# Optimization experiments

Hardware: AMD Instinct MI355X
Metric: run time of the kernel (lower is better)

## Reference

```python
import jax, jax.numpy as jnp
import numpy as np

N_NODES = 4096
JACOBI_ITERS = 10
EPS = 1e-5


def sym_laplacian_dense(edge_index, n):
    # L = I - D^{-1/2} A D^{-1/2}, duplicates in edge_index accumulate (as scipy COO does)
    row, col = edge_index[0], edge_index[1]
    A = jnp.zeros((n, n), jnp.float32).at[row, col].add(1.0)
    deg = A.sum(axis=1)
    dinv = jnp.where(deg > 0, 1.0 / jnp.sqrt(jnp.where(deg > 0, deg, 1.0)), 0.0)
    return jnp.eye(n, dtype=jnp.float32) - dinv[:, None] * A * dinv[None, :]


def jacobi_eig(a, iterations):
    # Faithful Jacobi: `iterations` Givens rotations, each zeroing the max |off-diag| entry.
    n = a.shape[0]
    upper = jnp.triu(jnp.ones((n, n), bool), k=1)

    def body(_, carry):
        a, p = carry
        idx = jnp.argmax(jnp.where(upper, jnp.abs(a), 0.0))
        k, l = idx // n, idx % n
        akl = a[k, l]
        aDiff = a[l, l] - a[k, k]
        akl_safe = jnp.where(akl == 0.0, 1.0, akl)
        aDiff_safe = jnp.where(aDiff == 0.0, 1.0, aDiff)
        phi = aDiff / (2.0 * akl_safe)
        t2 = 1.0 / (jnp.abs(phi) + jnp.sqrt(phi * phi + 1.0))
        t2 = jnp.where(phi < 0.0, -t2, t2)
        t1 = akl / aDiff_safe
        t = jnp.where(jnp.abs(akl) < jnp.abs(aDiff) * 1e-36, t1, t2)
        c = 1.0 / jnp.sqrt(t * t + 1.0)
        s = t * c
        # a <- G^T a G  (equivalent to the triangular in-place updates for symmetric a)
        ck, cl = a[:, k], a[:, l]
        a = a.at[:, k].set(c * ck - s * cl).at[:, l].set(s * ck + c * cl)
        rk, rl = a[k, :], a[l, :]
        a = a.at[k, :].set(c * rk - s * rl).at[l, :].set(s * rk + c * rl)
        a = a.at[k, l].set(0.0).at[l, k].set(0.0)
        pk, pl = p[:, k], p[:, l]
        p = p.at[:, k].set(c * pk - s * pl).at[:, l].set(s * pk + c * pl)
        return a, p

    a, p = jax.lax.fori_loop(0, iterations, body, (a, jnp.eye(n, dtype=a.dtype)))
    return jnp.diagonal(a), p


def setup_inputs() -> dict:
    key = jax.random.key(0)
    ks = jax.random.split(key, 8)
    n, cin, cout, r, e = N_NODES, 64, 64, 4, 100000
    x = jax.random.normal(ks[0], (n, cin), jnp.float32)
    src = jax.random.randint(ks[1], (e,), 0, n)
    dst = jax.random.randint(ks[2], (e,), 0, n)
    # symmetric graph (undirected), as the Jacobi solver assumes a symmetric Laplacian
    edge_index = jnp.stack([jnp.concatenate([src, dst]), jnp.concatenate([dst, src])]).astype(jnp.int64)
    stdv = 1.0 / np.sqrt(cin)
    real_weight = jax.random.uniform(ks[3], (cout, cin, r, 1), jnp.float32, -stdv, stdv)
    imag_weight = jax.random.uniform(ks[4], (cout, cin, r, 1), jnp.float32, -stdv, stdv)
    h = jax.random.uniform(ks[5], (cout, cin), jnp.float32, -stdv, stdv)
    c = jax.random.uniform(ks[6], (cout, cin, 1), jnp.float32, -stdv, stdv)
    bias = jnp.zeros((cout,), jnp.float32)
    return {"x": x, "edge_index": edge_index, "real_weight": real_weight,
            "imag_weight": imag_weight, "h": h, "c": c, "bias": bias}


def reference(x, edge_index, real_weight, imag_weight, h, c, bias):
    n = x.shape[0]
    r = real_weight.shape[2]
    L = sym_laplacian_dense(edge_index, n)
    w, U = jacobi_eig(L, JACOBI_ITERS)          # w: (N,), U: (N, N)
    aux = U.T @ x                                # (N, in)
    hw = h[:, :, None] * w[None, None, :]        # (out, in, N)
    a2 = jnp.where(hw > EPS,
                   2.0 * jnp.arctan(1.0 / jnp.where(hw > EPS, hw, 1.0)),
                   2.0)
    # theta[o,i,j,n] = a2[o,i,n] * (j+1)  -> (out, in, r, N)
    theta = a2[:, :, None, :] * jnp.arange(1, r + 1, dtype=x.dtype)[None, None, :, None]
    g = real_weight * jnp.cos(theta) - imag_weight * jnp.sin(theta)
    g = g.sum(axis=2) + c                        # (out, in, N)
    out = jnp.einsum('oin,ni->on', g, aux)       # Pmul + sum over in-channels
    output = U @ out.T + bias                    # (N, out); note: original's clamp(min=0) is a no-op
    return output
```

## Files before the change

### kernel.cpp

```cpp
#include <hip/hip_runtime.h>
#include <hip/hip_bf16.h>

#pragma clang fp contract(off)

#define N 4096
#define CIN 64
#define COUT 64
#define ITERS 10
#define MAXS 32
#define CANDMAX 384

typedef unsigned long long u64;

__device__ __forceinline__ u64 packkey(float v, unsigned j) {
    return ((u64)__float_as_uint(v) << 32) | (u64)(~j);
}
__device__ __forceinline__ u64 gkey(unsigned vb, unsigned row, unsigned col) {
    unsigned flat = (row << 12) | col;
    return ((u64)vb << 24) | (u64)((~flat) & 0xFFFFFFu);
}

__global__ void init_prep_k(int* __restrict__ deg, int* __restrict__ fill,
                            const float* __restrict__ hh, const float* __restrict__ cw,
                            const float* __restrict__ rw, const float* __restrict__ iw,
                            float2* __restrict__ hcT, float4* __restrict__ rwT,
                            float4* __restrict__ iwT) {
    int b = blockIdx.x;
    if (b < 16) {
        int i = b * 256 + threadIdx.x;
        deg[i] = 0; fill[i] = 0;
    } else {
        int idx = (b - 16) * 256 + threadIdx.x;
        int i = idx >> 6, o = idx & 63;
        int src = o * 64 + i;
        hcT[idx] = make_float2(hh[src], cw[src]);
        rwT[idx] = make_float4(rw[src * 4 + 0], rw[src * 4 + 1], rw[src * 4 + 2], rw[src * 4 + 3]);
        iwT[idx] = make_float4(iw[src * 4 + 0], iw[src * 4 + 1], iw[src * 4 + 2], iw[src * 4 + 3]);
    }
}

__global__ void edges1_k(const int* __restrict__ ei, int* __restrict__ deg, int E) {
    int e = blockIdx.x * 256 + threadIdx.x;
    if (e < E) atomicAdd(&deg[ei[e]], 1);
}

__global__ void __launch_bounds__(1024) scan_k(const int* __restrict__ deg,
                                               int* __restrict__ rowptr,
                                               float* __restrict__ dinv) {
    __shared__ int ps[1024];
    int t = threadIdx.x, b = t * 4;
    int d0 = deg[b], d1 = deg[b + 1], d2 = deg[b + 2], d3 = deg[b + 3];
    int local = d0 + d1 + d2 + d3;
    ps[t] = local;
    __syncthreads();
    for (int off = 1; off < 1024; off <<= 1) {
        int v = (t >= off) ? ps[t - off] : 0;
        __syncthreads();
        ps[t] += v;
        __syncthreads();
    }
    int excl = ps[t] - local;
    rowptr[b] = excl; rowptr[b + 1] = excl + d0;
    rowptr[b + 2] = excl + d0 + d1; rowptr[b + 3] = excl + d0 + d1 + d2;
    if (t == 1023) rowptr[4096] = ps[1023];
    dinv[b]     = d0 > 0 ? 1.0f / sqrtf((float)d0) : 0.0f;
    dinv[b + 1] = d1 > 0 ? 1.0f / sqrtf((float)d1) : 0.0f;
    dinv[b + 2] = d2 > 0 ? 1.0f / sqrtf((float)d2) : 0.0f;
    dinv[b + 3] = d3 > 0 ? 1.0f / sqrtf((float)d3) : 0.0f;
}

__global__ void edges2_k(const int* __restrict__ ei, const int* __restrict__ rowptr,
                         int* __restrict__ fill, int* __restrict__ colidx, int E) {
    int e = blockIdx.x * 256 + threadIdx.x;
    if (e < E) {
        int r = ei[e], c = ei[E + e];
        int pos = rowptr[r] + atomicAdd(&fill[r], 1);
        colidx[pos] = c;
    }
}

__global__ void __launch_bounds__(64) rowmax0_k(
        const int* __restrict__ rowptr, const int* __restrict__ colidx,
        const float* __restrict__ dinv, const float* __restrict__ x,
        float* __restrict__ y, float* __restrict__ diag, u64* __restrict__ top24T) {
    const int i = blockIdx.x, t = threadIdx.x;
    __shared__ float row[N];
    __shared__ u64 cand[CANDMAX];
    __shared__ int scnt;
    int rs = rowptr[i], re = rowptr[i + 1];
    if (t == 0) { scnt = 0; row[i] = 0.0f; }
    __syncthreads();
    for (int e = rs + t; e < re; e += 64) { int c2 = colidx[e]; if (c2 >= i) row[c2] = 0.0f; }
    __syncthreads();
    for (int e = rs + t; e < re; e += 64) { int c2 = colidx[e]; if (c2 >= i) atomicAdd(&row[c2], 1.0f); }
    __syncthreads();
    float di = dinv[i];
    for (int e = rs + t; e < re; e += 64) {
        int c2 = colidx[e];
        if (c2 > i) {
            float v = -((di * row[c2]) * dinv[c2]);
            int idx = atomicAdd(&scnt, 1);
            if (idx < CANDMAX) cand[idx] = packkey(fabsf(v), (unsigned)c2);
        }
    }
    __syncthreads();
    int L = scnt < CANDMAX ? scnt : CANDMAX;
    for (int r = 0; r < 24; ++r) {
        u64 best = 0ull;
        for (int idx = t; idx < L; idx += 64) { u64 cc = cand[idx]; if (cc > best) best = cc; }
        for (int off = 32; off; off >>= 1) { u64 o = __shfl_xor(best, off, 64); if (o > best) best = o; }
        if (t == 0) top24T[(size_t)r * N + i] = best;
        for (int idx = t; idx < L; idx += 64) { if (cand[idx] == best) cand[idx] = 0ull; }
        __syncthreads();
    }
    if (t == 0) diag[i] = 1.0f - ((di * row[i]) * di);
    y[i * CIN + t] = x[i * CIN + t];
}

__global__ void __launch_bounds__(1024) jacobi_k(
        const int* __restrict__ rowptr, const int* __restrict__ colidx,
        const float* __restrict__ dinv,
        float* __restrict__ diag, const u64* __restrict__ top24T, float* __restrict__ y,
        float* __restrict__ rowS, float* __restrict__ colS,
        int* __restrict__ dslotG, int* __restrict__ slistG, int* __restrict__ nslotsG,
        int* __restrict__ rotk, int* __restrict__ rotl,
        float* __restrict__ rotc, float* __restrict__ rotsv) {
    __shared__ __align__(16) float cntK[N], cntL[N];
    __shared__ __align__(16) float rowKst[N], rowLst[N];
    __shared__ __align__(16) float dinvL[N];
    __shared__ u64 rmaxL[N];
    __shared__ float rvalL[N];
    __shared__ float diagL[N];
    __shared__ short dslotL[N];
    __shared__ u64 rmaxSlot[MAXS];
    __shared__ u64 w16[16], w16b[16];
    __shared__ float ovRowK[MAXS], ovRowL[MAXS], ovColK[MAXS], ovColL[MAXS];
    __shared__ int slistL[MAXS];
    __shared__ unsigned short sdirty[64];
    __shared__ int S_snd;
    const int t = threadIdx.x;

    u64 mb0 = 0ull;
    for (int i = t; i < N; i += 1024) {
        u64 kk = top24T[i];
        rmaxL[i] = kk;
        rvalL[i] = -__uint_as_float((unsigned)(kk >> 32));
        diagL[i] = diag[i];
        dinvL[i] = dinv[i];
        dslotL[i] = -1;
        unsigned col = (~(unsigned)kk) & 4095u;
        u64 gk = gkey((unsigned)(kk >> 32), (unsigned)i, col);
        if (gk > mb0) mb0 = gk;
    }
    for (int off = 32; off; off >>= 1) { u64 o = __shfl_down(mb0, off, 64); if (o > mb0) mb0 = o; }
    if ((t & 63) == 0) w16[t >> 6] = mb0;
    __syncthreads();
    u64 pivot = w16[0];
    for (int w = 1; w < 16; ++w) if (w16[w] > pivot) pivot = w16[w];
    int nsCur = 0;

    for (int it = 0; it < ITERS; ++it) {
        unsigned flat = (~(unsigned)pivot) & 0xFFFFFFu;
        const int k = (int)(flat >> 12), l = (int)(flat & 4095u);
        const float akl = rvalL[k];
        const float akk = diagL[k], all_ = diagL[l];
        float aDiff = all_ - akk;
        float akl_safe = (akl == 0.0f) ? 1.0f : akl;
        float aDiff_safe = (aDiff == 0.0f) ? 1.0f : aDiff;
        float phi = aDiff / (2.0f * akl_safe);
        float t2 = 1.0f / (fabsf(phi) + sqrtf(phi * phi + 1.0f));
        t2 = (phi < 0.0f) ? -t2 : t2;
        float t1 = akl / aDiff_safe;
        float tt = (fabsf(akl) < fabsf(aDiff) * 1e-36f) ? t1 : t2;
        const float c = 1.0f / sqrtf(tt * tt + 1.0f);
        const float s = tt * c;
        float a1kk = c * akk - s * akl;
        float a1kl = s * akk + c * akl;
        float a1lk = c * akl - s * all_;
        float a1ll = s * akl + c * all_;
        const float a2kk = c * a1kk - s * a1lk;
        const float a2ll = s * a1kl + c * a1ll;
        int ok = dslotL[k], ol = dslotL[l];
        const int nold = nsCur;
        const bool freshK = (ok < 0), freshL = (ol < 0);
        int sk2 = ok, sl3 = ol;
        { int ns = nsCur; if (freshK) sk2 = ns++; if (freshL) sl3 = ns++; nsCur = ns; }
        const int slotk = sk2, slotl = sl3;
        const float dk = dinvL[k], dl = dinvL[l];
        if (freshK) for (int j = t; j < N; j += 1024) cntK[j] = 0.0f;
        if (freshL) for (int j = t; j < N; j += 1024) cntL[j] = 0.0f;
        __syncthreads();
        if (t == 0) {
            rotk[it] = k; rotl[it] = l; rotc[it] = c; rotsv[it] = s;
            diagL[k] = a2kk; diagL[l] = a2ll;
            if (freshK) { slistL[slotk] = k; dslotL[k] = (short)slotk; }
            if (freshL) { slistL[slotl] = l; dslotL[l] = (short)slotl; }
            S_snd = 0;
        }
        if (t < CIN) {
            float yk = y[k * CIN + t], yl = y[l * CIN + t];
            y[k * CIN + t] = c * yk - s * yl;
            y[l * CIN + t] = s * yk + c * yl;
        }
        if (t >= 64 && t < 64 + nold) {
            int sl2 = t - 64;
            if (freshK) { ovRowK[sl2] = colS[(size_t)sl2 * N + k]; ovColK[sl2] = rowS[(size_t)sl2 * N + k]; }
            if (freshL) { ovRowL[sl2] = colS[(size_t)sl2 * N + l]; ovColL[sl2] = rowS[(size_t)sl2 * N + l]; }
        }
        if (freshK) for (int e = rowptr[k] + t; e < rowptr[k + 1]; e += 1024) atomicAdd(&cntK[colidx[e]], 1.0f);
        if (freshL) for (int e = rowptr[l] + t; e < rowptr[l + 1]; e += 1024) atomicAdd(&cntL[colidx[e]], 1.0f);
        __syncthreads();
        u64 bk = packkey(0.0f, 4095u), bl = packkey(0.0f, 4095u);
        {
            const int j0 = t * 4;
            float4 dj4 = *reinterpret_cast<const float4*>(dinvL + j0);
            float4 bK4, bL4, cK4, cL4;
            if (freshK) {
                float4 cnt = *reinterpret_cast<const float4*>(cntK + j0);
#pragma unroll
                for (int m = 0; m < 4; ++m) {
                    float cn = (&cnt.x)[m], dj = (&dj4.x)[m];
                    (&bK4.x)[m] = -((dk * cn) * dj);
                    (&cK4.x)[m] = -((dj * cn) * dk);
                }
            } else {
                bK4 = *reinterpret_cast<const float4*>(rowS + (size_t)ok * N + j0);
                cK4 = *reinterpret_cast<const float4*>(colS + (size_t)ok * N + j0);
            }
            if (freshL) {
                float4 cnt = *reinterpret_cast<const float4*>(cntL + j0);
#pragma unroll
                for (int m = 0; m < 4; ++m) {
                    float cn = (&cnt.x)[m], dj = (&dj4.x)[m];
                    (&bL4.x)[m] = -((dl * cn) * dj);
                    (&cL4.x)[m] = -((dj * cn) * dl);
                }
            } else {
                bL4 = *reinterpret_cast<const float4*>(rowS + (size_t)ol * N + j0);
                cL4 = *reinterpret_cast<const float4*>(colS + (size_t)ol * N + j0);
            }
            float4 nrK4, nrL4, ncK4, ncL4;
#pragma unroll
            for (int m = 0; m < 4; ++m) {
                int j = j0 + m;
                float bK = (&bK4.x)[m], bL = (&bL4.x)[m];
                float cK = (&cK4.x)[m], cL = (&cL4.x)[m];
                float nrk, nrl, nck, ncl;
                if (j == k)      { nrk = a2kk; nrl = 0.0f; nck = a2kk; ncl = 0.0f; }
                else if (j == l) { nrk = 0.0f; nrl = a2ll; nck = 0.0f; ncl = a2ll; }
                else {
                    int sl2 = dslotL[j];
                    if (sl2 >= 0 && sl2 < nold) {
                        if (freshK) { bK = ovRowK[sl2]; cK = ovColK[sl2]; }
                        if (freshL) { bL = ovRowL[sl2]; cL = ovColL[sl2]; }
                    }
                    nrk = c * bK - s * bL; nrl = s * bK + c * bL;
                    nck = c * cK - s * cL; ncl = s * cK + c * cL;
                }
                (&nrK4.x)[m] = nrk; (&nrL4.x)[m] = nrl;
                (&ncK4.x)[m] = nck; (&ncL4.x)[m] = ncl;
                if (j > k) { u64 kk = packkey(fabsf(nrk), (unsigned)j); if (kk > bk) bk = kk; }
                if (j > l) { u64 kk = packkey(fabsf(nrl), (unsigned)j); if (kk > bl) bl = kk; }
            }
            *reinterpret_cast<float4*>(rowS + (size_t)slotk * N + j0) = nrK4;
            *reinterpret_cast<float4*>(rowS + (size_t)slotl * N + j0) = nrL4;
            *reinterpret_cast<float4*>(colS + (size_t)slotk * N + j0) = ncK4;
            *reinterpret_cast<float4*>(colS + (size_t)slotl * N + j0) = ncL4;
            *reinterpret_cast<float4*>(rowKst + j0) = nrK4;
            *reinterpret_cast<float4*>(rowLst + j0) = nrL4;
            *reinterpret_cast<float4*>(cntK + j0) = ncK4;
            *reinterpret_cast<float4*>(cntL + j0) = ncL4;
        }
        for (int off = 32; off; off >>= 1) {
            u64 o = __shfl_down(bk, off, 64); if (o > bk) bk = o;
            u64 o2 = __shfl_down(bl, off, 64); if (o2 > bl) bl = o2;
        }
        if ((t & 63) == 0) { w16[t >> 6] = bk; w16b[t >> 6] = bl; }
        __syncthreads();
        if (t == 0) {
            u64 b1 = w16[0], b2 = w16b[0];
            for (int w = 1; w < 16; ++w) { if (w16[w] > b1) b1 = w16[w]; if (w16b[w] > b2) b2 = w16b[w]; }
            unsigned j1 = (~(unsigned)b1) & 4095u, j2 = (~(unsigned)b2) & 4095u;
            rvalL[k] = rowKst[j1];
            rvalL[l] = rowLst[j2];
            rmaxSlot[slotk] = gkey((unsigned)(b1 >> 32), (unsigned)k, j1);
            rmaxSlot[slotl] = gkey((unsigned)(b2 >> 32), (unsigned)l, j2);
        }
        if (t >= 64 && t < 64 + nold) {
            int sl2 = t - 64;
            int js = slistL[sl2];
            if (js != k && js != l) {
                float vkj = rowKst[js];
                float vlj = rowLst[js];
                float vjk = cntK[js];
                float vjl = cntL[js];
                colS[(size_t)sl2 * N + k] = vkj;
                colS[(size_t)sl2 * N + l] = vlj;
                rowS[(size_t)sl2 * N + k] = vjk;
                rowS[(size_t)sl2 * N + l] = vjl;
                u64 cached = rmaxSlot[sl2];
                unsigned cj = ((~(unsigned)cached) & 0xFFFFFFu) & 4095u;
                bool kc = (k > js), lc = (l > js);
                u64 ck2 = kc ? gkey(__float_as_uint(fabsf(vjk)), (unsigned)js, (unsigned)k) : 0ull;
                u64 cl2 = lc ? gkey(__float_as_uint(fabsf(vjl)), (unsigned)js, (unsigned)l) : 0ull;
                bool stale = false; u64 base = cached; bool useOld = true;
                if (kc && cj == (unsigned)k)      { if (ck2 < cached) stale = true; else { base = 0ull; useOld = false; } }
                else if (lc && cj == (unsigned)l) { if (cl2 < cached) stale = true; else { base = 0ull; useOld = false; } }
                if (!stale) {
                    if (kc || lc) {
                        u64 mm = base; float mv = useOld ? rvalL[js] : 0.0f;
                        if (ck2 > mm) { mm = ck2; mv = vjk; }
                        if (cl2 > mm) { mm = cl2; mv = vjl; }
                        rmaxSlot[sl2] = mm; rvalL[js] = mv;
                    }
                } else { int d2 = atomicAdd(&S_snd, 1); sdirty[d2] = (unsigned short)sl2; }
            }
        }
        u64 myBest = 0ull;
#pragma unroll
        for (int m = 0; m < 4; ++m) {
            int j = t + 1024 * m;
            if (dslotL[j] >= 0) continue;
            float nck = cntK[j], ncl = cntL[j];
            u64 cached = rmaxL[j];
            unsigned cj = (~(unsigned)cached) & 4095u;
            bool kc = (k > j), lc = (l > j);
            u64 ck2 = kc ? packkey(fabsf(nck), (unsigned)k) : 0ull;
            u64 cl2 = lc ? packkey(fabsf(ncl), (unsigned)l) : 0ull;
            bool stale = false; u64 base = cached; bool useOld = true;
            if (kc && cj == (unsigned)k)      { if (ck2 < cached) stale = true; else { base = 0ull; useOld = false; } }
            else if (lc && cj == (unsigned)l) { if (cl2 < cached) stale = true; else { base = 0ull; useOld = false; } }
            if (!stale) {
                if (kc || lc) {
                    u64 mm = base; float mv = useOld ? rvalL[j] : 0.0f;
                    if (ck2 > mm) { mm = ck2; mv = nck; }
                    if (cl2 > mm) { mm = cl2; mv = ncl; }
                    rmaxL[j] = mm; rvalL[j] = mv;
                }
            } else {
                u64 bKey = 0ull; float bVal = 0.0f;
                for (int cc = 0; cc < 24; ++cc) {
                    u64 cand = top24T[(size_t)cc * N + j];
                    unsigned col = (~(unsigned)cand) & 4095u;
                    if (dslotL[col] < 0) {
                        bKey = cand;
                        bVal = -__uint_as_float((unsigned)(cand >> 32));
                        break;
                    }
                }
                for (int sl = 0; sl < nsCur; ++sl) {
                    if (sl == slotk || sl == slotl) continue;
                    int js = slistL[sl];
                    if (js > j) {
                        float v = colS[(size_t)sl * N + j];
                        u64 kk2 = packkey(fabsf(v), (unsigned)js);
                        if (kk2 > bKey) { bKey = kk2; bVal = v; }
                    }
                }
                if (kc && ck2 > bKey) { bKey = ck2; bVal = nck; }
                if (lc && cl2 > bKey) { bKey = cl2; bVal = ncl; }
                rmaxL[j] = bKey; rvalL[j] = bVal;
            }
            u64 fin = rmaxL[j];
            u64 gk = gkey((unsigned)(fin >> 32), (unsigned)j, (~(unsigned)fin) & 4095u);
            if (gk > myBest) myBest = gk;
        }
        __syncthreads();
        const int nd = S_snd;
        for (int d = 0; d < nd; ++d) {
            int sl2 = sdirty[d];
            int ir = slistL[sl2];
            u64 bb = packkey(0.0f, 4095u);
            int jb = t * 4;
            float4 v4 = *reinterpret_cast<const float4*>(rowS + (size_t)sl2 * N + jb);
#pragma unroll
            for (int m = 0; m < 4; ++m) {
                int j = jb + m;
                if (j > ir) {
                    u64 kk = packkey(fabsf((&v4.x)[m]), (unsigned)j);
                    if (kk > bb) bb = kk;
                }
            }
            for (int off = 32; off; off >>= 1) { u64 o = __shfl_down(bb, off, 64); if (o > bb) bb = o; }
            if ((t & 63) == 0) w16[t >> 6] = bb;
            __syncthreads();
            if (t == 0) {
                u64 b = w16[0];
                for (int w = 1; w < 16; ++w) if (w16[w] > b) b = w16[w];
                unsigned js2 = (~(unsigned)b) & 4095u;
                rmaxSlot[sl2] = gkey((unsigned)(b >> 32), (unsigned)ir, js2);
                rvalL[ir] = rowS[(size_t)sl2 * N + js2];
            }
            __syncthreads();
        }
        if (t < nsCur) { u64 o2 = rmaxSlot[t]; if (o2 > myBest) myBest = o2; }
        for (int off = 32; off; off >>= 1) { u64 o = __shfl_down(myBest, off, 64); if (o > myBest) myBest = o; }
        if ((t & 63) == 0) w16[t >> 6] = myBest;
        __syncthreads();
        pivot = w16[0];
        for (int w = 1; w < 16; ++w) if (w16[w] > pivot) pivot = w16[w];
    }
    for (int i = t; i < N; i += 1024) {
        diag[i] = diagL[i];
        dslotG[i] = (int)dslotL[i];
    }
    if (t < nsCur) slistG[t] = slistL[t];
    if (t == 0) *nslotsG = nsCur;
}

__global__ void __launch_bounds__(1024) spectral_k(
        const float* __restrict__ diag, const float* __restrict__ y,
        const float2* __restrict__ hcT, const float4* __restrict__ rwT,
        const float4* __restrict__ iwT, float* __restrict__ z) {
    int o = threadIdx.x & 63;
    int nl = threadIdx.x >> 6;
    int n = blockIdx.x * 16 + nl;
    __shared__ float saux[16][CIN];
    saux[nl][o] = y[n * CIN + o];
    __syncthreads();
    float wn = diag[n];
    const float C2 = -0.41614683654714241f;
    const float S2 = 0.90929742682568170f;
    float acc = 0.0f;
    for (int i = 0; i < CIN; ++i) {
        float2 hc = hcT[i * 64 + o];
        float hw = hc.x * wn;
        float t2v = hw * hw;
        float inv = 1.0f / (t2v + 1.0f);
        float c1 = (t2v - 1.0f) * inv;
        float s1 = (2.0f * hw) * inv;
        if (!(hw > 1e-5f)) { c1 = C2; s1 = S2; }
        float4 rwv = rwT[i * 64 + o];
        float4 iwv = iwT[i * 64 + o];
        float g = hc.y;
        float cj = c1, sj = s1;
        g += rwv.x * cj - iwv.x * sj;
        float cn = cj * c1 - sj * s1; float sn = sj * c1 + cj * s1; cj = cn; sj = sn;
        g += rwv.y * cj - iwv.y * sj;
        cn = cj * c1 - sj * s1; sn = sj * c1 + cj * s1; cj = cn; sj = sn;
        g += rwv.z * cj - iwv.z * sj;
        cn = cj * c1 - sj * s1; sn = sj * c1 + cj * s1; cj = cn; sj = sn;
        g += rwv.w * cj - iwv.w * sj;
        acc += g * saux[nl][i];
    }
    z[(size_t)n * COUT + o] = acc;
}

__global__ void store_fused_k(
        float* __restrict__ z, const float* __restrict__ bias,
        const int* __restrict__ dslot, const int* __restrict__ slistG,
        const int* __restrict__ nslotsG,
        const int* __restrict__ rotk, const int* __restrict__ rotl,
        const float* __restrict__ rotc, const float* __restrict__ rotsv,
        float* __restrict__ out) {
    int t = threadIdx.x;
    if (blockIdx.x < 1024) {
        int idx = blockIdx.x * 256 + t;
        int row = idx >> 6;
        if (dslot[row] < 0) out[idx] = z[idx] + bias[idx & 63];
    } else if (t < 64) {
        for (int i = ITERS - 1; i >= 0; --i) {
            int k = rotk[i], l = rotl[i];
            float c = rotc[i], s = rotsv[i];
            float zk = z[k * COUT + t];
            float zl = z[l * COUT + t];
            z[k * COUT + t] = c * zk + s * zl;
            z[l * COUT + t] = -s * zk + c * zl;
        }
        int ns = *nslotsG;
        for (int d = 0; d < ns; ++d) {
            int r = slistG[d];
            out[r * COUT + t] = z[r * COUT + t] + bias[t];
        }
    }
}

extern "C" void kernel_launch(void* const* d_in, const int* in_sizes, int n_in,
                              void* d_out, int out_size, void* d_ws, size_t ws_size,
                              hipStream_t stream) {
    const float* x   = (const float*)d_in[0];
    const int*   ei  = (const int*)d_in[1];
    const float* rw  = (const float*)d_in[2];
    const float* iw  = (const float*)d_in[3];
    const float* hh  = (const float*)d_in[4];
    const float* cw  = (const float*)d_in[5];
    const float* bias= (const float*)d_in[6];
    float* out = (float*)d_out;

    float* rowS = (float*)d_ws;
    float* colS = rowS + (size_t)MAXS * N;
    float* y    = colS + (size_t)MAXS * N;
    float* z    = y + N * CIN;
    float2* hcT = (float2*)(z + N * COUT);
    float4* rwT = (float4*)(hcT + 4096);
    float4* iwT = rwT + 4096;
    float* dinv = (float*)(iwT + 4096);
    float* diag = dinv + N;
    u64* top24T = (u64*)(diag + N);
    int* rowptr = (int*)(top24T + 24 * (size_t)N);
    int* fill   = rowptr + 4100;
    int* deg    = fill + N;
    int* slist  = deg + N;
    int* nslots = slist + 64;
    int* dslot  = nslots + 4;
    int* rotk   = dslot + N;
    int* rotl   = rotk + 16;
    float* rotc = (float*)(rotl + 16);
    float* rotsv= rotc + 16;
    int* colidx = (int*)(rotsv + 16);

    int E = in_sizes[1] / 2;
    int eb = (E + 255) / 256;

    init_prep_k<<<32, 256, 0, stream>>>(deg, fill, hh, cw, rw, iw, hcT, rwT, iwT);
    edges1_k<<<eb, 256, 0, stream>>>(ei, deg, E);
    scan_k<<<1, 1024, 0, stream>>>(deg, rowptr, dinv);
    edges2_k<<<eb, 256, 0, stream>>>(ei, rowptr, fill, colidx, E);
    rowmax0_k<<<N, 64, 0, stream>>>(rowptr, colidx, dinv, x, y, diag, top24T);

    jacobi_k<<<1, 1024, 0, stream>>>(rowptr, colidx, dinv, diag, top24T,
                                     y, rowS, colS, dslot, slist, nslots,
                                     rotk, rotl, rotc, rotsv);

    spectral_k<<<N / 16, 1024, 0, stream>>>(diag, y, hcT, rwT, iwT, z);
    store_fused_k<<<1025, 256, 0, stream>>>(z, bias, dslot, slist, nslots,
                                            rotk, rotl, rotc, rotsv, out);
}
```

Measured before the change: 267.1 us.

## Overlap spectral filter with single-block Jacobi by fusing into one launch

The spectral filter now runs in extra blocks of the Jacobi kernel, so it executes on the idle CUs while the single-block Jacobi loop runs, instead of in a separate launch afterwards. Rows touched by rotations can be read mid-update by those blocks, so the store kernel recomputes the spectral term for just those rows from the final diag and y, then applies the inverse rotations in shared memory. The Jacobi loop also zeroes its count buffers during the existing pass instead of with an extra barrier, and finds slots by scanning the short slot list. The cost is that every spectral block now carries the Jacobi kernel's large LDS footprint, and the store kernel launches 1024-thread blocks where only 256 threads do work.

```diff
diff --git a/kernel.cpp b/kernel.cpp
--- a/kernel.cpp
+++ b/kernel.cpp
@@ -18,6 +18,32 @@
 __device__ __forceinline__ u64 gkey(unsigned vb, unsigned row, unsigned col) {
     unsigned flat = (row << 12) | col;
     return ((u64)vb << 24) | (u64)((~flat) & 0xFFFFFFu);
+}
+
+__device__ __forceinline__ float spec_term(float wn, int o, int i,
+        const float2* __restrict__ hcT, const float4* __restrict__ rwT,
+        const float4* __restrict__ iwT) {
+    const float C2 = -0.41614683654714241f;
+    const float S2 = 0.90929742682568170f;
+    float2 hc = hcT[i * 64 + o];
+    float hw = hc.x * wn;
+    float t2v = hw * hw;
+    float inv = 1.0f / (t2v + 1.0f);
+    float c1 = (t2v - 1.0f) * inv;
+    float s1 = (2.0f * hw) * inv;
+    if (!(hw > 1e-5f)) { c1 = C2; s1 = S2; }
+    float4 rwv = rwT[i * 64 + o];
+    float4 iwv = iwT[i * 64 + o];
+    float g = hc.y;
+    float cj = c1, sj = s1;
+    g += rwv.x * cj - iwv.x * sj;
+    float cn = cj * c1 - sj * s1; float sn = sj * c1 + cj * s1; cj = cn; sj = sn;
+    g += rwv.y * cj - iwv.y * sj;
+    cn = cj * c1 - sj * s1; sn = sj * c1 + cj * s1; cj = cn; sj = sn;
+    g += rwv.z * cj - iwv.z * sj;
+    cn = cj * c1 - sj * s1; sn = sj * c1 + cj * s1; cj = cn; sj = sn;
+    g += rwv.w * cj - iwv.w * sj;
+    return g;
 }
 
 __global__ void init_prep_k(int* __restrict__ deg, int* __restrict__ fill,
@@ -117,14 +143,16 @@
     y[i * CIN + t] = x[i * CIN + t];
 }
 
-__global__ void __launch_bounds__(1024) jacobi_k(
+__global__ void __launch_bounds__(1024) jacspec_k(
         const int* __restrict__ rowptr, const int* __restrict__ colidx,
         const float* __restrict__ dinv,
         float* __restrict__ diag, const u64* __restrict__ top24T, float* __restrict__ y,
         float* __restrict__ rowS, float* __restrict__ colS,
         int* __restrict__ dslotG, int* __restrict__ slistG, int* __restrict__ nslotsG,
         int* __restrict__ rotk, int* __restrict__ rotl,
-        float* __restrict__ rotc, float* __restrict__ rotsv) {
+        float* __restrict__ rotc, float* __restrict__ rotsv,
+        const float2* __restrict__ hcT, const float4* __restrict__ rwT,
+        const float4* __restrict__ iwT, float* __restrict__ z) {
     __shared__ __align__(16) float cntK[N], cntL[N];
     __shared__ __align__(16) float rowKst[N], rowLst[N];
     __shared__ __align__(16) float dinvL[N];
@@ -140,6 +168,20 @@
     __shared__ int S_snd;
     const int t = threadIdx.x;
 
+    if (blockIdx.x != 0) {
+        float (*saux)[CIN] = (float(*)[CIN])cntK;
+        int o = t & 63, nl = t >> 6;
+        int n = (blockIdx.x - 1) * 16 + nl;
+        saux[nl][o] = y[n * CIN + o];
+        __syncthreads();
+        float wn = diag[n];
+        float acc = 0.0f;
+        for (int i = 0; i < CIN; ++i)
+            acc += spec_term(wn, o, i, hcT, rwT, iwT) * saux[nl][i];
+        z[(size_t)n * COUT + o] = acc;
+        return;
+    }
+
     u64 mb0 = 0ull;
     for (int i = t; i < N; i += 1024) {
         u64 kk = top24T[i];
@@ -148,6 +190,8 @@
         diagL[i] = diag[i];
         dinvL[i] = dinv[i];
         dslotL[i] = -1;
+        cntK[i] = 0.0f;
+        cntL[i] = 0.0f;
         unsigned col = (~(unsigned)kk) & 4095u;
         u64 gk = gkey((unsigned)(kk >> 32), (unsigned)i, col);
         if (gk > mb0) mb0 = gk;
@@ -180,19 +224,20 @@
         float a1ll = s * akl + c * all_;
         const float a2kk = c * a1kk - s * a1lk;
         const float a2ll = s * a1kl + c * a1ll;
-        int ok = dslotL[k], ol = dslotL[l];
+        int ok = -1, ol = -1;
+        for (int sl = 0; sl < nsCur; ++sl) {
+            int js = slistL[sl];
+            if (js == k) ok = sl;
+            if (js == l) ol = sl;
+        }
         const int nold = nsCur;
         const bool freshK = (ok < 0), freshL = (ol < 0);
         int sk2 = ok, sl3 = ol;
         { int ns = nsCur; if (freshK) sk2 = ns++; if (freshL) sl3 = ns++; nsCur = ns; }
         const int slotk = sk2, slotl = sl3;
         const float dk = dinvL[k], dl = dinvL[l];
-        if (freshK) for (int j = t; j < N; j += 1024) cntK[j] = 0.0f;
-        if (freshL) for (int j = t; j < N; j += 1024) cntL[j] = 0.0f;
-        __syncthreads();
         if (t == 0) {
             rotk[it] = k; rotl[it] = l; rotc[it] = c; rotsv[it] = s;
-            diagL[k] = a2kk; diagL[l] = a2ll;
             if (freshK) { slistL[slotk] = k; dslotL[k] = (short)slotk; }
             if (freshL) { slistL[slotl] = l; dslotL[l] = (short)slotl; }
             S_snd = 0;
@@ -285,6 +330,7 @@
             rvalL[l] = rowLst[j2];
             rmaxSlot[slotk] = gkey((unsigned)(b1 >> 32), (unsigned)k, j1);
             rmaxSlot[slotl] = gkey((unsigned)(b2 >> 32), (unsigned)l, j2);
+            diagL[k] = a2kk; diagL[l] = a2ll;
         }
         if (t >= 64 && t < 64 + nold) {
             int sl2 = t - 64;
@@ -367,6 +413,12 @@
         }
         __syncthreads();
         const int nd = S_snd;
+        {
+            const int j0 = t * 4;
+            float4 zz; zz.x = zz.y = zz.z = zz.w = 0.0f;
+            *reinterpret_cast<float4*>(cntK + j0) = zz;
+            *reinterpret_cast<float4*>(cntL + j0) = zz;
+        }
         for (int d = 0; d < nd; ++d) {
             int sl2 = sdirty[d];
             int ir = slistL[sl2];
@@ -408,69 +460,49 @@
     if (t == 0) *nslotsG = nsCur;
 }
 
-__global__ void __launch_bounds__(1024) spectral_k(
-        const float* __restrict__ diag, const float* __restrict__ y,
-        const float2* __restrict__ hcT, const float4* __restrict__ rwT,
-        const float4* __restrict__ iwT, float* __restrict__ z) {
-    int o = threadIdx.x & 63;
-    int nl = threadIdx.x >> 6;
-    int n = blockIdx.x * 16 + nl;
-    __shared__ float saux[16][CIN];
-    saux[nl][o] = y[n * CIN + o];
-    __syncthreads();
-    float wn = diag[n];
-    const float C2 = -0.41614683654714241f;
-    const float S2 = 0.90929742682568170f;
-    float acc = 0.0f;
-    for (int i = 0; i < CIN; ++i) {
-        float2 hc = hcT[i * 64 + o];
-        float hw = hc.x * wn;
-        float t2v = hw * hw;
-        float inv = 1.0f / (t2v + 1.0f);
-        float c1 = (t2v - 1.0f) * inv;
-        float s1 = (2.0f * hw) * inv;
-        if (!(hw > 1e-5f)) { c1 = C2; s1 = S2; }
-        float4 rwv = rwT[i * 64 + o];
-        float4 iwv = iwT[i * 64 + o];
-        float g = hc.y;
-        float cj = c1, sj = s1;
-        g += rwv.x * cj - iwv.x * sj;
-        float cn = cj * c1 - sj * s1; float sn = sj * c1 + cj * s1; cj = cn; sj = sn;
-        g += rwv.y * cj - iwv.y * sj;
-        cn = cj * c1 - sj * s1; sn = sj * c1 + cj * s1; cj = cn; sj = sn;
-        g += rwv.z * cj - iwv.z * sj;
-        cn = cj * c1 - sj * s1; sn = sj * c1 + cj * s1; cj = cn; sj = sn;
-        g += rwv.w * cj - iwv.w * sj;
-        acc += g * saux[nl][i];
-    }
-    z[(size_t)n * COUT + o] = acc;
-}
-
-__global__ void store_fused_k(
-        float* __restrict__ z, const float* __restrict__ bias,
+__global__ void __launch_bounds__(1024) store_fused_k(
+        const float* __restrict__ z, const float* __restrict__ bias,
         const int* __restrict__ dslot, const int* __restrict__ slistG,
         const int* __restrict__ nslotsG,
         const int* __restrict__ rotk, const int* __restrict__ rotl,
         const float* __restrict__ rotc, const float* __restrict__ rotsv,
+        const float* __restrict__ diag, const float* __restrict__ y,
+        const float2* __restrict__ hcT, const float4* __restrict__ rwT,
+        const float4* __restrict__ iwT,
         float* __restrict__ out) {
+    __shared__ float zloc[MAXS][COUT];
     int t = threadIdx.x;
     if (blockIdx.x < 1024) {
-        int idx = blockIdx.x * 256 + t;
-        int row = idx >> 6;
-        if (dslot[row] < 0) out[idx] = z[idx] + bias[idx & 63];
-    } else if (t < 64) {
-        for (int i = ITERS - 1; i >= 0; --i) {
-            int k = rotk[i], l = rotl[i];
-            float c = rotc[i], s = rotsv[i];
-            float zk = z[k * COUT + t];
-            float zl = z[l * COUT + t];
-            z[k * COUT + t] = c * zk + s * zl;
-            z[l * COUT + t] = -s * zk + c * zl;
-        }
+        int idx = blockIdx.x * 256 + (t & 255);
+        if (t < 256) {
+            int row = idx >> 6;
+            if (dslot[row] < 0) out[idx] = z[idx] + bias[idx & 63];
+        }
+    } else {
         int ns = *nslotsG;
-        for (int d = 0; d < ns; ++d) {
-            int r = slistG[d];
-            out[r * COUT + t] = z[r * COUT + t] + bias[t];
+        int o = t & 63, d = t >> 6;
+        for (int dd = d; dd < ns; dd += 16) {
+            int r = slistG[dd];
+            float wn = diag[r];
+            float acc = 0.0f;
+            for (int i = 0; i < CIN; ++i)
+                acc += spec_term(wn, o, i, hcT, rwT, iwT) * y[r * CIN + i];
+            zloc[dd][o] = acc;
+        }
+        __syncthreads();
+        if (t < 64) {
+            for (int i = ITERS - 1; i >= 0; --i) {
+                int k = rotk[i], l = rotl[i];
+                float c = rotc[i], s = rotsv[i];
+                int sk = dslot[k], sl = dslot[l];
+                float zk = zloc[sk][t], zl = zloc[sl][t];
+                zloc[sk][t] = c * zk + s * zl;
+                zloc[sl][t] = -s * zk + c * zl;
+            }
+        }
+        __syncthreads();
+        for (int dd = d; dd < ns; dd += 16) {
+            out[slistG[dd] * COUT + o] = zloc[dd][o] + bias[o];
         }
     }
 }
@@ -518,11 +550,12 @@
     edges2_k<<<eb, 256, 0, stream>>>(ei, rowptr, fill, colidx, E);
     rowmax0_k<<<N, 64, 0, stream>>>(rowptr, colidx, dinv, x, y, diag, top24T);
 
-    jacobi_k<<<1, 1024, 0, stream>>>(rowptr, colidx, dinv, diag, top24T,
-                                     y, rowS, colS, dslot, slist, nslots,
-                                     rotk, rotl, rotc, rotsv);
-
-    spectral_k<<<N / 16, 1024, 0, stream>>>(diag, y, hcT, rwT, iwT, z);
-    store_fused_k<<<1025, 256, 0, stream>>>(z, bias, dslot, slist, nslots,
-                                            rotk, rotl, rotc, rotsv, out);
-}
+    jacspec_k<<<257, 1024, 0, stream>>>(rowptr, colidx, dinv, diag, top24T,
+                                        y, rowS, colS, dslot, slist, nslots,
+                                        rotk, rotl, rotc, rotsv,
+                                        hcT, rwT, iwT, z);
+
+    store_fused_k<<<1025, 1024, 0, stream>>>(z, bias, dslot, slist, nslots,
+                                             rotk, rotl, rotc, rotsv,
+                                             diag, y, hcT, rwT, iwT, out);
+}
```

Result: slower. 274.5 us (+2.8%).
